# Optimization experiments

Measured on AMD Instinct MI355X. Metric: run time of the kernel, lower is better.

## Reference

```python
import jax, jax.numpy as jnp
import numpy as np

B, H, L, CHUNK, D = 2, 8, 32, 64, 64
MAX_REL = 32
N = L * CHUNK


def setup_inputs() -> dict:
    key = jax.random.key(0)
    k1, k2, k3 = jax.random.split(key, 3)
    x = jax.random.normal(k1, (B, H, N, D), dtype=jnp.float32)
    pos = jax.random.randint(k2, (B, L, L), 0, 64, dtype=jnp.int64)
    # xavier_uniform-like init for the embeddings table
    table_shape = (2 * MAX_REL + 1, D)
    limit = np.sqrt(6.0 / (table_shape[0] + table_shape[1])).astype(np.float32)
    embeddings_table = jax.random.uniform(
        k3, table_shape, dtype=jnp.float32, minval=-limit, maxval=limit)
    return {"x": x, "pos": pos, "embeddings_table": embeddings_table,
            "chunk_size": CHUNK}


def reference(x, pos, embeddings_table, chunk_size):
    # x: [b,h,N,d], pos: [b,l,l], embeddings_table: [2*mrp+1, d]
    mrp = (embeddings_table.shape[0] - 1) // 2
    idx = jnp.clip(pos, -mrp, mrp) + mrp            # [b,l,l]
    emb = embeddings_table[idx]                      # [b,l,l,d] gather
    b, h, n_tot, d = x.shape
    l = pos.shape[1]
    n = chunk_size
    assert n_tot == l * n
    # '(l n)' split: l outer blocks, n inner positions
    xc = x.reshape(b, h, l, n, d)                    # [b,h,q,n,d]
    # per-chunk dot products: row block q, col block k, row offset n
    scores = jnp.einsum('bhqnd,bqkd->bhqnk', xc, emb)  # [b,h,l,n,l]
    # broadcast over inner column offset m (value independent of m)
    out = jnp.broadcast_to(scores[..., None], (b, h, l, n, l, n))
    return out.reshape(b, h, n_tot, n_tot)           # [b,h,N,N]
```

## Files before the change

kernel.cpp:

```cpp
#include <hip/hip_runtime.h>

#define BB 2
#define HH 8
#define LL 32
#define CHK 64
#define DD 64
#define MAX_REL 32
#define NN 2048

__global__ __launch_bounds__(256) void relpos_kernel(
    const float* __restrict__ x,
    const int*   __restrict__ pos,
    const float* __restrict__ table,
    float*       __restrict__ out)
{
    const int row = blockIdx.x;
    const int n_  = row & (NN - 1);
    const int bh  = row >> 11;
    const int b   = bh >> 3;
    const int q   = n_ >> 6;

    const int t    = threadIdx.x;
    const int k    = t >> 3;
    const int part = t & 7;

    int p = pos[(b * LL + q) * LL + k];
    p = min(max(p, -MAX_REL), MAX_REL) + MAX_REL;

    const float* erow = table + (size_t)p * DD + part * 8;
    const float* xrow = x + (size_t)row * DD + part * 8;

    float4 xa = *(const float4*)(xrow);
    float4 xb = *(const float4*)(xrow + 4);
    float4 ea = *(const float4*)(erow);
    float4 eb = *(const float4*)(erow + 4);

    float s = xa.x * ea.x + xa.y * ea.y + xa.z * ea.z + xa.w * ea.w
            + xb.x * eb.x + xb.y * eb.y + xb.z * eb.z + xb.w * eb.w;

    s += __shfl_xor(s, 1);
    s += __shfl_xor(s, 2);
    s += __shfl_xor(s, 4);

    __shared__ float sk[32];
    if (part == 0) sk[k] = s;
    __syncthreads();

    float4* orow = (float4*)(out + (size_t)row * NN);
    #pragma unroll
    for (int j = 0; j < 2; ++j) {
        int c4 = t + j * 256;
        float v = sk[c4 >> 4];
        orow[c4] = make_float4(v, v, v, v);
    }
}

extern "C" void kernel_launch(void* const* d_in, const int* in_sizes, int n_in,
                              void* d_out, int out_size, void* d_ws, size_t ws_size,
                              hipStream_t stream) {
    const float* x     = (const float*)d_in[0];
    const int*   pos   = (const int*)d_in[1];
    const float* table = (const float*)d_in[2];
    float*       out   = (float*)d_out;

    dim3 grid(BB * HH * NN);
    relpos_kernel<<<grid, 256, 0, stream>>>(x, pos, table, out);
}
```

Measured before the change: 61.68 us.

## Process eight rows per wavefront, reuse embedding gathers, use nontemporal stores

```diff
diff --git a/kernel.cpp b/kernel.cpp
--- a/kernel.cpp
+++ b/kernel.cpp
@@ -7,6 +7,9 @@
 #define DD 64
 #define MAX_REL 32
 #define NN 2048
+#define RPW 8
+
+typedef float f32x4 __attribute__((ext_vector_type(4)));
 
 __global__ __launch_bounds__(256) void relpos_kernel(
     const float* __restrict__ x,
@@ -14,44 +17,59 @@
     const float* __restrict__ table,
     float*       __restrict__ out)
 {
-    const int row = blockIdx.x;
-    const int n_  = row & (NN - 1);
-    const int bh  = row >> 11;
-    const int b   = bh >> 3;
-    const int q   = n_ >> 6;
+    const int wid  = blockIdx.x * 4 + (threadIdx.x >> 6);
+    const int lane = threadIdx.x & 63;
+    const int part = lane & 7;
+    const int kgrp = lane >> 3;
 
-    const int t    = threadIdx.x;
-    const int k    = t >> 3;
-    const int part = t & 7;
+    const int row0 = wid * RPW;
+    const int q    = (row0 >> 6) & (LL - 1);
+    const int b    = row0 >> 14;
 
-    int p = pos[(b * LL + q) * LL + k];
-    p = min(max(p, -MAX_REL), MAX_REL) + MAX_REL;
+    f32x4 ea[4], eb[4];
+    const int pbase = (b * LL + q) * LL;
+    #pragma unroll
+    for (int p = 0; p < 4; ++p) {
+        int pp = pos[pbase + p * 8 + kgrp];
+        pp = min(max(pp, -MAX_REL), MAX_REL) + MAX_REL;
+        const float* erow = table + pp * DD + part * 8;
+        ea[p] = *(const f32x4*)(erow);
+        eb[p] = *(const f32x4*)(erow + 4);
+    }
 
-    const float* erow = table + (size_t)p * DD + part * 8;
-    const float* xrow = x + (size_t)row * DD + part * 8;
+    const float* xbase = x + (size_t)row0 * DD + part * 8;
 
-    float4 xa = *(const float4*)(xrow);
-    float4 xb = *(const float4*)(xrow + 4);
-    float4 ea = *(const float4*)(erow);
-    float4 eb = *(const float4*)(erow + 4);
+    f32x4 xa = *(const f32x4*)(xbase);
+    f32x4 xb = *(const f32x4*)(xbase + 4);
 
-    float s = xa.x * ea.x + xa.y * ea.y + xa.z * ea.z + xa.w * ea.w
-            + xb.x * eb.x + xb.y * eb.y + xb.z * eb.z + xb.w * eb.w;
+    for (int r = 0; r < RPW; ++r) {
+        const f32x4 cxa = xa, cxb = xb;
+        if (r + 1 < RPW) {
+            xa = *(const f32x4*)(xbase + (r + 1) * DD);
+            xb = *(const f32x4*)(xbase + (r + 1) * DD + 4);
+        }
 
-    s += __shfl_xor(s, 1);
-    s += __shfl_xor(s, 2);
-    s += __shfl_xor(s, 4);
+        float s[4];
+        #pragma unroll
+        for (int p = 0; p < 4; ++p) {
+            float t = cxa.x * ea[p].x + cxa.y * ea[p].y
+                    + cxa.z * ea[p].z + cxa.w * ea[p].w
+                    + cxb.x * eb[p].x + cxb.y * eb[p].y
+                    + cxb.z * eb[p].z + cxb.w * eb[p].w;
+            t += __shfl_xor(t, 1);
+            t += __shfl_xor(t, 2);
+            t += __shfl_xor(t, 4);
+            s[p] = t;
+        }
 
-    __shared__ float sk[32];
-    if (part == 0) sk[k] = s;
-    __syncthreads();
-
-    float4* orow = (float4*)(out + (size_t)row * NN);
-    #pragma unroll
-    for (int j = 0; j < 2; ++j) {
-        int c4 = t + j * 256;
-        float v = sk[c4 >> 4];
-        orow[c4] = make_float4(v, v, v, v);
+        float* orow = out + (size_t)(row0 + r) * NN;
+        #pragma unroll
+        for (int j = 0; j < 8; ++j) {
+            int src = ((4 * j + (lane >> 4)) & 7) << 3;
+            float v = __shfl(s[j >> 1], src);
+            f32x4 v4 = {v, v, v, v};
+            __builtin_nontemporal_store(v4, (f32x4*)orow + j * 64 + lane);
+        }
     }
 }
 
@@ -63,6 +81,6 @@
     const float* table = (const float*)d_in[2];
     float*       out   = (float*)d_out;
 
-    dim3 grid(BB * HH * NN);
+    dim3 grid(BB * HH * NN / RPW / 4);
     relpos_kernel<<<grid, 256, 0, stream>>>(x, pos, table, out);
 }
```

Result: faster. 54.76 us (-11.2%).
